# Kernel tuning notes

Hardware: AMD Instinct MI355X
Metric: run time of the kernel (lower is better)

The kernel has to match this reference:

```python
import jax, jax.numpy as jnp
import numpy as np
from math import factorial, sqrt, pi

MUL = 8
LS = [0, 1, 2]                       # l values for both Rs_in and Rs_out
RS = [(MUL, l) for l in LS]
N_NODES = 20000
N_EDGES = 100000
FEAT = sum(m * (2 * l + 1) for m, l in RS)       # 72
R_TOT = sum(mo * mi * (2 * min(lo, li) + 1) for mo, lo in RS for mi, li in RS)  # 1216
L_MAX = max(LS) + max(LS)            # 4
RSH_DIM = (L_MAX + 1) ** 2           # 25
NB, H = 10, 100                      # radial basis size / hidden width
MIN_R, MAX_R = 0.7, 3.2
SWISH_SCALE = 1.679177               # e3nn rescaled swish factor


def _w3j_entry(j1, j2, j3, m1, m2, m3):
    # complex-basis Wigner 3j (Racah formula)
    if m1 + m2 + m3 != 0 or not (abs(j1 - j2) <= j3 <= j1 + j2):
        return 0.0
    t1, t2 = j2 - m1 - j3, j1 + m2 - j3
    kmin, kmax = max(0, t1, t2), min(j1 + j2 - j3, j1 - m1, j2 + m2)
    s = sum((-1) ** k / (factorial(k) * factorial(k - t1) * factorial(k - t2)
                         * factorial(j1 + j2 - j3 - k) * factorial(j1 - m1 - k) * factorial(j2 + m2 - k))
            for k in range(kmin, kmax + 1))
    pref = (-1) ** (j1 - j2 - m3) * sqrt(
        factorial(j1 + j2 - j3) * factorial(j1 - j2 + j3) * factorial(-j1 + j2 + j3) / factorial(j1 + j2 + j3 + 1)
        * factorial(j1 + m1) * factorial(j1 - m1) * factorial(j2 + m2) * factorial(j2 - m2)
        * factorial(j3 + m3) * factorial(j3 - m3))
    return pref * s


def _real_cob(l):
    # complex->real spherical-harmonic change of basis
    U = np.zeros((2 * l + 1, 2 * l + 1), dtype=complex)
    U[l, l] = 1.0
    s = 1.0 / np.sqrt(2.0)
    for m in range(1, l + 1):
        U[l + m, l + m] = (-1) ** m * s
        U[l + m, l - m] = s
        U[l - m, l - m] = 1j * s
        U[l - m, l + m] = -1j * ((-1) ** m) * s
    return U


def _wigner3j_real(l1, l2, l3):
    w = np.zeros((2 * l1 + 1, 2 * l2 + 1, 2 * l3 + 1))
    for m1 in range(-l1, l1 + 1):
        for m2 in range(-l2, l2 + 1):
            m3 = -m1 - m2
            if abs(m3) <= l3:
                w[m1 + l1, m2 + l2, m3 + l3] = _w3j_entry(l1, l2, l3, m1, m2, m3)
    T = np.einsum('am,bn,cp,mnp->abc', _real_cob(l1), _real_cob(l2), _real_cob(l3), w.astype(complex))
    C = T.real if np.linalg.norm(T.real) >= np.linalg.norm(T.imag) else T.imag
    n = np.linalg.norm(C)
    return (C / n if n > 0 else C).astype(np.float32)


# precomputed constants (coupling coefficients + normalization), as in MinimalNetwork.__init__
C3 = {(lo, li, lf): jnp.asarray(_wigner3j_real(lo, li, lf))
      for _, lo in RS for _, li in RS for lf in range(abs(lo - li), lo + li + 1)}


def _norm_coef():
    nc = np.zeros((len(RS), len(RS)), dtype=np.float32)
    for i, (_, lo) in enumerate(RS):
        num = sum(mi * (2 * min(lo, li) + 1) for mi, li in RS)
        nc[i, :] = sqrt(4 * pi) * sqrt(2 * lo + 1) / sqrt(num)
    return jnp.asarray(nc)

NORM = _norm_coef()


def _swish(x):
    return SWISH_SCALE * x * jax.nn.sigmoid(x)


def _radial(r, Ws):
    # GaussianRadialModel: gaussian basis -> 3 hidden swish layers -> linear out
    centers = jnp.linspace(MIN_R, MAX_R, NB)
    sigma = (MAX_R - MIN_R) / (NB - 1)
    x = jnp.exp(-(((r[:, None] - centers) / sigma) ** 2))
    for W in Ws[:-1]:
        x = _swish(x @ (W / jnp.sqrt(jnp.asarray(W.shape[0], x.dtype))))
    W = Ws[-1]
    return x @ (W / jnp.sqrt(jnp.asarray(W.shape[0], x.dtype)))


def _tensor_message(F_src, rsh, R):
    # F_src: [E, FEAT] gathered source features; rsh: [E, 25]; R: [E, R_TOT]
    E = F_src.shape[0]
    f_offs = np.cumsum([0] + [m * (2 * l + 1) for m, l in RS])
    msgs, r_off = [], 0
    for i, (U, lo) in enumerate(RS):
        acc = jnp.zeros((E, U, 2 * lo + 1), F_src.dtype)
        for j, (V, li) in enumerate(RS):
            nlf = 2 * min(lo, li) + 1
            Rb = R[:, r_off:r_off + U * V * nlf].reshape(E, U, V, nlf)
            r_off += U * V * nlf
            Fb = F_src[:, f_offs[j]:f_offs[j + 1]].reshape(E, V, 2 * li + 1)
            for fi, lf in enumerate(range(abs(lo - li), lo + li + 1)):
                # K[e,mo,mi] = sum_mf C3[mo,mi,mf] * Y_lf[e,mf]
                K = jnp.einsum('oif,ef->eoi', C3[(lo, li, lf)], rsh[:, lf * lf:(lf + 1) * (lf + 1)])
                acc = acc + NORM[i, j] * jnp.einsum('eoi,evi,euv->euo', K, Fb, Rb[..., fi])
        msgs.append(acc.reshape(E, -1))
    return jnp.concatenate(msgs, axis=-1)


def _forward(features, edge_index, radii, rsh, Ws):
    R = _radial(radii, Ws)                                     # [E, R_TOT]
    msg = _tensor_message(features[edge_index[0]], rsh, R)     # [E, FEAT]
    # scatter-add aggregation at target nodes (MessagePassing aggr='add')
    return jnp.zeros((features.shape[0], msg.shape[1]), msg.dtype).at[edge_index[1]].add(msg)


def setup_inputs() -> dict:
    key = jax.random.key(0)
    ks = jax.random.split(key, 8)
    features = jax.random.normal(ks[0], (N_NODES, FEAT), jnp.float32)
    edge_index = jax.random.randint(ks[1], (2, N_EDGES), 0, N_NODES)
    radii = MIN_R + (MAX_R - MIN_R) * jax.random.uniform(ks[2], (N_EDGES,), jnp.float32)
    rsh = jax.random.normal(ks[3], (N_EDGES, RSH_DIM), jnp.float32)
    W0 = jax.random.normal(ks[4], (NB, H), jnp.float32)
    W1 = jax.random.normal(ks[5], (H, H), jnp.float32)
    W2 = jax.random.normal(ks[6], (H, H), jnp.float32)
    W3 = jax.random.normal(ks[7], (H, R_TOT), jnp.float32)
    return {"features": features, "edge_index": edge_index, "radii": radii, "rsh": rsh,
            "W0": W0, "W1": W1, "W2": W2, "W3": W3}


def reference(features, edge_index, radii, rsh, W0, W1, W2, W3):
    return _forward(features, edge_index, radii, rsh, (W0, W1, W2, W3))
```

## Files before the change

kernel.cpp:

```cpp
#include <hip/hip_runtime.h>
#include <hip/hip_bf16.h>
#include <math.h>


#define FEATD 72
#define NCOL 1216
#define SWISH_SCALE 1.679177f

typedef __attribute__((ext_vector_type(8))) short bf16x8;
typedef __attribute__((ext_vector_type(4))) float f32x4;

constexpr int NCOMBO = 19;
constexpr int CB_LO[NCOMBO] = {0,0,0,1,1,1,1,1,1,1,2,2,2,2,2,2,2,2,2};
constexpr int CB_LI[NCOMBO] = {0,1,2,0,1,1,1,2,2,2,0,1,1,1,2,2,2,2,2};
constexpr int CB_LF[NCOMBO] = {0,1,2,1,0,1,2,1,2,3,2,1,2,3,0,1,2,3,4};
constexpr int CB_OFF[NCOMBO] = {0,1,10,35,44,53,80,125,170,245,350,375,420,495,600,625,700,825,1000};
constexpr int CB_SZ[NCOMBO]  = {1,9,25,9,9,27,45,45,75,105,25,45,75,105,25,75,125,175,225};
constexpr int C3TOT = 1225;

constexpr int C3OFFT[3][3][5] = {
  { {0,-1,-1,-1,-1}, {-1,1,-1,-1,-1}, {-1,-1,10,-1,-1} },
  { {-1,35,-1,-1,-1}, {44,53,80,-1,-1}, {-1,125,170,245,-1} },
  { {-1,-1,350,-1,-1}, {-1,375,420,495,-1}, {600,625,700,825,1000} }
};
constexpr int ROFFT[3][3] = {{0,64,128},{192,256,448},{640,704,896}};
constexpr int FOFFT[3]   = {0,8,32};

__device__ const double d_fact[11] = {1.,1.,2.,6.,24.,120.,720.,5040.,40320.,362880.,3628800.};

__device__ double w3j_entry(int j1,int j2,int j3,int m1,int m2,int m3){
  if (m1+m2+m3 != 0) return 0.0;
  int dj = j1-j2; if (dj<0) dj=-dj;
  if (j3 < dj || j3 > j1+j2) return 0.0;
  int t1 = j2 - m1 - j3, t2 = j1 + m2 - j3;
  int kmin = 0; if (t1>kmin) kmin=t1; if (t2>kmin) kmin=t2;
  int kmax = j1+j2-j3; if (j1-m1<kmax) kmax=j1-m1; if (j2+m2<kmax) kmax=j2+m2;
  double s = 0.0;
  for (int k=kmin;k<=kmax;++k){
    double den = d_fact[k]*d_fact[k-t1]*d_fact[k-t2]*d_fact[j1+j2-j3-k]
               * d_fact[j1-m1-k]*d_fact[j2+m2-k];
    s += ((k&1)? -1.0:1.0)/den;
  }
  double pref = sqrt(d_fact[j1+j2-j3]*d_fact[j1-j2+j3]*d_fact[-j1+j2+j3]/d_fact[j1+j2+j3+1]
               * d_fact[j1+m1]*d_fact[j1-m1]*d_fact[j2+m2]*d_fact[j2-m2]
               * d_fact[j3+m3]*d_fact[j3-m3]);
  int ex = j1-j2-m3;
  if (ex & 1) pref = -pref;
  return pref*s;
}

__device__ void cob(int l, int r, int c, double& re, double& im){
  re = 0.0; im = 0.0;
  int mr = r - l, mc = c - l;
  const double s = 0.70710678118654752440;
  if (mr == 0) { if (mc == 0) re = 1.0; return; }
  if (mr > 0) {
    if (mc == mr)       re = (mr & 1) ? -s : s;
    else if (mc == -mr) re = s;
  } else {
    int m = -mr;
    if (mc == -m)      im = s;
    else if (mc == m)  im = (m & 1) ? s : -s;
  }
}

__global__ void c3_build_kernel(double* __restrict__ Tre, double* __restrict__ Tim){
  int idx = blockIdx.x*64 + threadIdx.x;
  if (idx >= C3TOT) return;
  int c = 0;
  while (c+1 < NCOMBO && idx >= CB_OFF[c+1]) ++c;
  int lo = CB_LO[c], li = CB_LI[c], lf = CB_LF[c];
  int n2 = 2*li+1, n3 = 2*lf+1;
  int loc = idx - CB_OFF[c];
  int a = loc/(n2*n3), b = (loc/n3)%n2, g = loc%n3;
  double sre=0.0, sim=0.0;
  for (int m1=-lo; m1<=lo; ++m1){
    for (int m2=-li; m2<=li; ++m2){
      int m3 = -m1-m2;
      if (m3 < -lf || m3 > lf) continue;
      double w = w3j_entry(lo,li,lf,m1,m2,m3);
      if (w == 0.0) continue;
      double r1,i1,r2,i2,r3,i3;
      cob(lo, a, m1+lo, r1,i1);
      cob(li, b, m2+li, r2,i2);
      cob(lf, g, m3+lf, r3,i3);
      double rr = r1*r2 - i1*i2, ri = r1*i2 + i1*r2;
      double fr = rr*r3 - ri*i3, fi = rr*i3 + ri*r3;
      sre += fr*w; sim += fi*w;
    }
  }
  Tre[idx] = sre; Tim[idx] = sim;
}

__global__ void c3_norm_kernel(const double* __restrict__ Tre, const double* __restrict__ Tim,
                               float* __restrict__ C3f){
  int c = blockIdx.x;
  int off = CB_OFF[c], sz = CB_SZ[c];
  int t = threadIdx.x;
  double sre=0.0, sim=0.0;
  for (int p=t; p<sz; p+=64){ double x=Tre[off+p], y=Tim[off+p]; sre+=x*x; sim+=y*y; }
  for (int m=1; m<64; m<<=1){ sre += __shfl_xor(sre, m, 64); sim += __shfl_xor(sim, m, 64); }
  bool useRe = (sre >= sim);
  double n = sqrt(useRe ? sre : sim);
  double inv = (n > 0.0) ? 1.0/n : 1.0;
  for (int p=t; p<sz; p+=64){
    double v = useRe ? Tre[off+p] : Tim[off+p];
    C3f[off+p] = (float)(v*inv);
  }
}

__global__ __launch_bounds__(256) void prep_w3t_kernel(const float* __restrict__ W3,
                                                       __hip_bfloat16* __restrict__ W3t){
  int idx = blockIdx.x*256 + threadIdx.x;
  if (idx >= 1216*136) return;
  int cp = idx/136, k = idx%136;
  int chunk = cp>>6, uv = cp&63;
  int lo = CB_LO[chunk], li = CB_LI[chunk], lf = CB_LF[chunk];
  int lmin = lo<li ? lo : li;
  int nlf = 2*lmin+1;
  int fi = lf - (lo>li ? lo-li : li-lo);
  int c = ROFFT[lo][li] + uv*nlf + fi;
  float v = (k < 100) ? 0.1f*W3[(size_t)k*NCOL + c] : 0.f;
  W3t[idx] = __float2bfloat16(v);
}

__global__ __launch_bounds__(256) void prep_wt_kernel(const float* __restrict__ W1,
                                                      const float* __restrict__ W2,
                                                      __hip_bfloat16* __restrict__ W1t,
                                                      __hip_bfloat16* __restrict__ W2t){
  int idx = blockIdx.x*256 + threadIdx.x;
  constexpr int HALF = 112*136;
  if (idx >= 2*HALF) return;
  const float* W = (idx < HALF) ? W1 : W2;
  __hip_bfloat16* Wt = (idx < HALF) ? W1t : W2t;
  int r = (idx < HALF) ? idx : idx - HALF;
  int o = r/136, k = r%136;
  float v = (o < 100 && k < 100) ? 0.1f*W[k*100+o] : 0.f;
  Wt[r] = __float2bfloat16(v);
}

__device__ __forceinline__ float swishf(float s){
  return SWISH_SCALE * s / (1.f + __expf(-s));
}

__device__ __forceinline__ void radial_layer_mfma(
    const __hip_bfloat16* __restrict__ sIn,
    const __hip_bfloat16* __restrict__ Wt,
    __hip_bfloat16* __restrict__ sOut,
    int wv, int lr, int lq)
{
  bf16x8 bf[4];
  #pragma unroll
  for (int ks=0; ks<4; ++ks)
    bf[ks] = *(const bf16x8*)&sIn[(wv*16+lr)*136 + ks*32 + lq*8];
  f32x4 acc[7] = {};
  #pragma unroll
  for (int ks=0; ks<4; ++ks)
    #pragma unroll
    for (int ot=0; ot<7; ++ot){
      bf16x8 a = *(const bf16x8*)&Wt[(ot*16+lr)*136 + ks*32 + lq*8];
      acc[ot] = __builtin_amdgcn_mfma_f32_16x16x32_bf16(a, bf[ks], acc[ot], 0, 0, 0);
    }
  #pragma unroll
  for (int ot=0; ot<7; ++ot){
    __hip_bfloat16 hv[4];
    #pragma unroll
    for (int r=0; r<4; ++r)
      hv[r] = __float2bfloat16(swishf(acc[ot][r]));
    *(short4*)&sOut[(wv*16+lr)*136 + ot*16 + lq*4] = *(short4*)hv;
  }
  {
    int lane = lq*16 + lr;
    int row = lane & 15, q = lane >> 4;
    short4 z = {0,0,0,0};
    *(short4*)&sOut[(wv*16+row)*136 + 112 + q*4] = z;
  }
}

__global__ __launch_bounds__(256,4) void radial_mfma_kernel(
    const float* __restrict__ radii, const float* __restrict__ W0,
    const __hip_bfloat16* __restrict__ W1t, const __hip_bfloat16* __restrict__ W2t,
    __hip_bfloat16* __restrict__ h_bf, int E)
{
  __shared__ float sbas[640];
  __shared__ __align__(16) __hip_bfloat16 sA[64*136];
  __shared__ __align__(16) __hip_bfloat16 sB[64*136];
  const int t = threadIdx.x;
  const int et0 = blockIdx.x*64;

  for (int p=t; p<640; p+=256){
    int er = p/10, k = p%10;
    int eg = et0 + er;
    float r = (eg < E) ? radii[eg] : 0.f;
    float c = 0.7f + (2.5f/9.0f)*(float)k;
    float d = (r - c) * (9.0f/2.5f);
    sbas[p] = __expf(-d*d);
  }
  __syncthreads();
  for (int p=t; p<6400; p+=256){
    int er = p/100, o = p%100;
    float s = 0.f;
    #pragma unroll
    for (int k=0;k<10;++k) s += sbas[er*10+k]*W0[k*100+o];
    sA[er*136+o] = __float2bfloat16(swishf(s*0.3162277660168379f));
  }
  for (int p=t; p<64*36; p+=256){
    int er = p/36, k = 100 + p%36;
    sA[er*136+k] = __float2bfloat16(0.f);
  }
  __syncthreads();

  const int lane = t & 63, wv = t >> 6;
  const int lr = lane & 15, lq = lane >> 4;

  radial_layer_mfma(sA, W1t, sB, wv, lr, lq);
  __builtin_amdgcn_wave_barrier();
  radial_layer_mfma(sB, W2t, sA, wv, lr, lq);
  __builtin_amdgcn_wave_barrier();
  {
    const float4* sm = (const float4*)(sA + (size_t)(wv*16)*136);
    float4* gm = (float4*)(h_bf + (size_t)(et0 + wv*16)*136);
    for (int p=lane; p<272; p+=64) gm[p] = sm[p];
  }
}

__global__ __launch_bounds__(256) void hist_kernel(const int* __restrict__ ei,
                                                   int* __restrict__ deg, int E){
  int e = blockIdx.x*256 + threadIdx.x;
  if (e < E) atomicAdd(&deg[ei[E+e]], 1);
}

__global__ __launch_bounds__(256) void scan_kernel(const int* __restrict__ deg,
                                                   int* __restrict__ off,
                                                   int* __restrict__ cursor, int N, int E){
  __shared__ int part[256], spref[256];
  const int t = threadIdx.x;
  const int CH = (N + 255)/256;
  int lo = t*CH, hi = lo+CH < N ? lo+CH : N;
  int s = 0;
  for (int n=lo; n<hi; ++n) s += deg[n];
  part[t] = s;
  __syncthreads();
  if (t == 0){
    int run = 0;
    for (int i=0;i<256;++i){ spref[i] = run; run += part[i]; }
  }
  __syncthreads();
  int run = spref[t];
  for (int n=lo; n<hi; ++n){ off[n] = run; cursor[n] = run; run += deg[n]; }
  if (t == 255) off[N] = E;
}

__global__ __launch_bounds__(256) void fill_kernel(const int* __restrict__ ei,
                                                   int* __restrict__ cursor,
                                                   int* __restrict__ eid, int E){
  int e = blockIdx.x*256 + threadIdx.x;
  if (e < E){
    int idx = atomicAdd(&cursor[ei[E+e]], 1);
    eid[idx] = e;
  }
}

__global__ __launch_bounds__(64) void gather_kernel(const float* __restrict__ msg,
                                                    const int* __restrict__ off,
                                                    const int* __restrict__ eid,
                                                    float* __restrict__ out, int N){
  const int n = blockIdx.x;
  const int t = threadIdx.x;
  const int s = off[n], e1 = off[n+1];
  float a0 = 0.f, a1 = 0.f;
  for (int i=s; i<e1; ++i){
    const float* m = msg + (size_t)eid[i]*FEATD;
    a0 += m[t];
    if (t < 8) a1 += m[64+t];
  }
  out[(size_t)n*FEATD + t] = a0;
  if (t < 8) out[(size_t)n*FEATD + 64 + t] = a1;
}

constexpr int OF_RT  = 0;
constexpr int OF_ACC = 17408;
constexpr int OF_F   = 27648;
constexpr int OF_KV  = 46080;
constexpr int OF_SRC = 52480;
constexpr int SMEM_SZ = 52736;

template<int LO,int LI,int LF>
__device__ __forceinline__ void phase(
    int chunk, const __hip_bfloat16* __restrict__ W3t, const bf16x8 (&hf)[4],
    float* sRt, float* sFf, float* sKV,
    const float* __restrict__ C3g, const float* __restrict__ rshrow,
    float* sAcc, int t)
{
  constexpr int NO = 2*LO+1, NI = 2*LI+1, NF = 2*LF+1;
  constexpr int C3B = C3OFFT[LO][LI][LF];
  constexpr int FO  = FOFFT[LI];

  const int e = t >> 2, role = t & 3;
  const int lane = t & 63, wv = t >> 6;
  const int lr = lane & 15, lq = lane >> 4;

  {
    float y[NF];
    #pragma unroll
    for (int mf=0; mf<NF; ++mf) y[mf] = rshrow[LF*LF + mf];
    for (int it = role; it < NO*NI; it += 4){
      float s = 0.f;
      #pragma unroll
      for (int mf=0; mf<NF; ++mf) s += C3g[C3B + it*NF + mf] * y[mf];
      sKV[e*25 + it] = s;
    }
  }
  {
    const __hip_bfloat16* wb = W3t + (size_t)chunk*64*136;
    f32x4 a4[4] = {};
    #pragma unroll
    for (int ks=0; ks<4; ++ks){
      #pragma unroll
      for (int ct=0; ct<4; ++ct){
        bf16x8 a = *(const bf16x8*)&wb[(ct*16+lr)*136 + ks*32 + lq*8];
        a4[ct] = __builtin_amdgcn_mfma_f32_16x16x32_bf16(a, hf[ks], a4[ct], 0, 0, 0);
      }
    }
    #pragma unroll
    for (int ct=0; ct<4; ++ct)
      *(f32x4*)&sRt[(wv*16 + lr)*68 + ct*16 + lq*4] = a4[ct];
  }
  __builtin_amdgcn_wave_barrier();

  {
    float H[2][NI];
    #pragma unroll
    for (int du=0; du<2; ++du)
      #pragma unroll
      for (int mi=0; mi<NI; ++mi) H[du][mi] = 0.f;

    #pragma unroll
    for (int vg=0; vg<2; ++vg){
      float fb[4*NI];
      #pragma unroll
      for (int p=0; p<NI; ++p)
        *(f32x4*)&fb[p*4] = *(const f32x4*)&sFf[e*72 + FO + vg*4*NI + p*4];
      #pragma unroll
      for (int du=0; du<2; ++du){
        const int u = role*2 + du;
        f32x4 rv = *(const f32x4*)&sRt[e*68 + u*8 + vg*4];
        #pragma unroll
        for (int v=0; v<4; ++v)
          #pragma unroll
          for (int mi=0; mi<NI; ++mi)
            H[du][mi] += rv[v] * fb[v*NI + mi];
      }
    }
    const int u0 = role*2, u1 = role*2 + 1;
    const int b0 = e*40 + ((LO==0) ? u0 : (LO==1) ? u0*3 : u0*5);
    const int b1 = e*40 + ((LO==0) ? u1 : (LO==1) ? u1*3 : u1*5);
    #pragma unroll
    for (int o=0; o<NO; ++o){
      float s0 = 0.f, s1 = 0.f;
      #pragma unroll
      for (int mi=0; mi<NI; ++mi){
        float kvv = sKV[e*25 + o*NI + mi];
        s0 += kvv * H[0][mi];
        s1 += kvv * H[1][mi];
      }
      sAcc[b0 + o] += s0;
      sAcc[b1 + o] += s1;
    }
  }
  __builtin_amdgcn_wave_barrier();
}

template<int J0,int W>
__device__ __forceinline__ void flush_group(float* sAcc, float* __restrict__ msg,
                                            int eb, int t, float nrm)
{
  const int lane = t & 63, wv = t >> 6;
  __builtin_amdgcn_wave_barrier();
  for (int p = lane; p < 16*W; p += 64){
    int el = wv*16 + p/W, j = p%W;
    msg[(size_t)(eb + el)*FEATD + J0 + j] = nrm * sAcc[el*40 + j];
    sAcc[el*40 + j] = 0.f;
  }
  __builtin_amdgcn_wave_barrier();
}

__global__ __launch_bounds__(256,3) void fused_kernel(
    const float* __restrict__ feats, const int* __restrict__ ei,
    const float* __restrict__ rsh, const __hip_bfloat16* __restrict__ h_bf,
    const __hip_bfloat16* __restrict__ W3t, const float* __restrict__ C3g,
    float* __restrict__ msg, int E)
{
  __shared__ __align__(16) char smem[SMEM_SZ];
  float* sRt  = (float*)(smem + OF_RT);
  float* sAcc = (float*)(smem + OF_ACC);
  float* sFf  = (float*)(smem + OF_F);
  float* sKV  = (float*)(smem + OF_KV);
  int*   sSrc = (int*)(smem + OF_SRC);

  const int t = threadIdx.x;
  const int eb = blockIdx.x*64;

  bf16x8 hf[4];
  {
    const int lane = t & 63, wv = t >> 6;
    const int lr = lane & 15, lq = lane >> 4;
    const __hip_bfloat16* hrow = h_bf + (size_t)(eb + wv*16 + lr)*136;
    #pragma unroll
    for (int ks=0; ks<4; ++ks)
      hf[ks] = *(const bf16x8*)&hrow[ks*32 + lq*8];
  }
  for (int p=t; p<2560; p+=256) sAcc[p] = 0.f;
  for (int p=t; p<64; p+=256){
    int e = eb + p;
    sSrc[p] = (e < E) ? ei[e] : 0;
  }
  __syncthreads();
  for (int p=t; p<64*72; p+=256){
    int el = p/72, j = p%72;
    sFf[el*72 + j] = feats[(size_t)sSrc[el]*72 + j];
  }
  __syncthreads();

  int eg = eb + (t >> 2); if (eg > E-1) eg = E-1;
  const float* rshrow = rsh + (size_t)eg*25;

  phase<0,0,0>( 0, W3t, hf, sRt, sFf, sKV, C3g, rshrow, sAcc, t);
  phase<0,1,1>( 1, W3t, hf, sRt, sFf, sKV, C3g, rshrow, sAcc, t);
  phase<0,2,2>( 2, W3t, hf, sRt, sFf, sKV, C3g, rshrow, sAcc, t);
  flush_group<0,8>(sAcc, msg, eb, t, 0.72360125f);

  phase<1,0,1>( 3, W3t, hf, sRt, sFf, sKV, C3g, rshrow, sAcc, t);
  phase<1,1,0>( 4, W3t, hf, sRt, sFf, sKV, C3g, rshrow, sAcc, t);
  phase<1,1,1>( 5, W3t, hf, sRt, sFf, sKV, C3g, rshrow, sAcc, t);
  phase<1,1,2>( 6, W3t, hf, sRt, sFf, sKV, C3g, rshrow, sAcc, t);
  phase<1,2,1>( 7, W3t, hf, sRt, sFf, sKV, C3g, rshrow, sAcc, t);
  phase<1,2,2>( 8, W3t, hf, sRt, sFf, sKV, C3g, rshrow, sAcc, t);
  phase<1,2,3>( 9, W3t, hf, sRt, sFf, sKV, C3g, rshrow, sAcc, t);
  flush_group<8,24>(sAcc, msg, eb, t, 0.8204867f);

  phase<2,0,2>(10, W3t, hf, sRt, sFf, sKV, C3g, rshrow, sAcc, t);
  phase<2,1,1>(11, W3t, hf, sRt, sFf, sKV, C3g, rshrow, sAcc, t);
  phase<2,1,2>(12, W3t, hf, sRt, sFf, sKV, C3g, rshrow, sAcc, t);
  phase<2,1,3>(13, W3t, hf, sRt, sFf, sKV, C3g, rshrow, sAcc, t);
  phase<2,2,0>(14, W3t, hf, sRt, sFf, sKV, C3g, rshrow, sAcc, t);
  phase<2,2,1>(15, W3t, hf, sRt, sFf, sKV, C3g, rshrow, sAcc, t);
  phase<2,2,2>(16, W3t, hf, sRt, sFf, sKV, C3g, rshrow, sAcc, t);
  phase<2,2,3>(17, W3t, hf, sRt, sFf, sKV, C3g, rshrow, sAcc, t);
  phase<2,2,4>(18, W3t, hf, sRt, sFf, sKV, C3g, rshrow, sAcc, t);
  flush_group<32,40>(sAcc, msg, eb, t, 0.9341652f);
}

extern "C" void kernel_launch(void* const* d_in, const int* in_sizes, int n_in,
                              void* d_out, int out_size, void* d_ws, size_t ws_size,
                              hipStream_t stream)
{
  const float* feats = (const float*)d_in[0];
  const int*   ei    = (const int*)d_in[1];
  const float* radii = (const float*)d_in[2];
  const float* rsh   = (const float*)d_in[3];
  const float* W0    = (const float*)d_in[4];
  const float* W1    = (const float*)d_in[5];
  const float* W2    = (const float*)d_in[6];
  const float* W3    = (const float*)d_in[7];
  float* out = (float*)d_out;
  const int E = in_sizes[2];
  const int N = in_sizes[0]/FEATD;

  const int EPAD = ((E + 63)/64)*64;
  const int NBLK = EPAD/64;

  char* ws = (char*)d_ws;
  size_t off_b = 0;
  float*  C3f = (float*)(ws + off_b);  off_b += 8192;
  double* Tre = (double*)(ws + off_b); off_b += 12288;
  double* Tim = (double*)(ws + off_b); off_b += 12288;
  __hip_bfloat16* W3t = (__hip_bfloat16*)(ws + off_b); off_b += 335872;
  __hip_bfloat16* W1t = (__hip_bfloat16*)(ws + off_b); off_b += 30720;
  __hip_bfloat16* W2t = (__hip_bfloat16*)(ws + off_b); off_b += 30720;
  __hip_bfloat16* h_bf = (__hip_bfloat16*)(ws + off_b); off_b += (size_t)EPAD*272;
  float* msg = (float*)(ws + off_b);   off_b += (size_t)EPAD*FEATD*4;
  int* deg    = (int*)(ws + off_b);    off_b += (size_t)N*4;
  int* offv   = (int*)(ws + off_b);    off_b += (size_t)(N+1)*4;
  int* cursor = (int*)(ws + off_b);    off_b += (size_t)N*4;
  int* eid    = (int*)(ws + off_b);    off_b += (size_t)E*4;

  c3_build_kernel<<<dim3((C3TOT+63)/64), dim3(64), 0, stream>>>(Tre, Tim);
  c3_norm_kernel<<<dim3(NCOMBO), dim3(64), 0, stream>>>(Tre, Tim, C3f);
  prep_w3t_kernel<<<dim3((1216*136+255)/256), dim3(256), 0, stream>>>(W3, W3t);
  prep_wt_kernel<<<dim3((2*112*136+255)/256), dim3(256), 0, stream>>>(W1, W2, W1t, W2t);

  hipMemsetAsync(deg, 0, (size_t)N*4, stream);
  hist_kernel<<<dim3((E+255)/256), dim3(256), 0, stream>>>(ei, deg, E);
  scan_kernel<<<dim3(1), dim3(256), 0, stream>>>(deg, offv, cursor, N, E);
  fill_kernel<<<dim3((E+255)/256), dim3(256), 0, stream>>>(ei, cursor, eid, E);

  radial_mfma_kernel<<<dim3(NBLK), dim3(256), 0, stream>>>(radii, W0, W1t, W2t, h_bf, E);
  fused_kernel<<<dim3(NBLK), dim3(256), 0, stream>>>(feats, ei, rsh, h_bf, W3t, C3f, msg, E);
  gather_kernel<<<dim3(N), dim3(64), 0, stream>>>(msg, offv, eid, out, N);
}
```

Measured before the change: 409.7 us.

## Stage W3 chunks into swizzled LDS via async global-to-LDS loads

Each phase now copies its 64x128 bf16 W3 chunk into shared memory with global_load_lds using an XOR-swizzled layout, and the MFMA A-fragments are read from LDS instead of global memory. The rsh rows and the C3 coefficients are also cached in shared memory once per block. The aim is to cut repeated global/L2 traffic and uncoalesced fragment loads, and to overlap the chunk copy with the KV computation. In exchange, two block-wide barriers are added per phase, LDS use grows to about 80 KB, and occupancy drops from 3 to 2 blocks per CU.

```diff
diff --git a/kernel.cpp b/kernel.cpp
--- a/kernel.cpp
+++ b/kernel.cpp
@@ -112,16 +112,17 @@
 __global__ __launch_bounds__(256) void prep_w3t_kernel(const float* __restrict__ W3,
                                                        __hip_bfloat16* __restrict__ W3t){
   int idx = blockIdx.x*256 + threadIdx.x;
-  if (idx >= 1216*136) return;
-  int cp = idx/136, k = idx%136;
-  int chunk = cp>>6, uv = cp&63;
+  if (idx >= 1216*128) return;
+  int cp = idx >> 7, k = idx & 127;
+  int chunk = cp >> 6, r = cp & 63;
   int lo = CB_LO[chunk], li = CB_LI[chunk], lf = CB_LF[chunk];
   int lmin = lo<li ? lo : li;
   int nlf = 2*lmin+1;
   int fi = lf - (lo>li ? lo-li : li-lo);
-  int c = ROFFT[lo][li] + uv*nlf + fi;
+  int c = ROFFT[lo][li] + r*nlf + fi;
   float v = (k < 100) ? 0.1f*W3[(size_t)k*NCOL + c] : 0.f;
-  W3t[idx] = __float2bfloat16(v);
+  int swz = (r*16 + (k>>3)) ^ (r&7);
+  W3t[(size_t)chunk*8192 + swz*8 + (k&7)] = __float2bfloat16(v);
 }
 
 __global__ __launch_bounds__(256) void prep_wt_kernel(const float* __restrict__ W1,
@@ -278,18 +279,35 @@
   if (t < 8) out[(size_t)n*FEATD + 64 + t] = a1;
 }
 
-constexpr int OF_RT  = 0;
-constexpr int OF_ACC = 17408;
-constexpr int OF_F   = 27648;
-constexpr int OF_KV  = 46080;
-constexpr int OF_SRC = 52480;
-constexpr int SMEM_SZ = 52736;
+constexpr int OF_W   = 0;
+constexpr int OF_RT  = 16384;
+constexpr int OF_ACC = 33792;
+constexpr int OF_F   = 44032;
+constexpr int OF_KV  = 62464;
+constexpr int OF_RSH = 68864;
+constexpr int OF_C3  = 75264;
+constexpr int OF_SRC = 80176;
+constexpr int SMEM_SZ = 80432;
+
+__device__ __forceinline__ void stage_chunk(const __hip_bfloat16* __restrict__ W3t,
+                                            int chunk, char* sW, int t)
+{
+  const int lane = t & 63, wv = t >> 6;
+  const char* g = (const char*)W3t + (size_t)chunk*16384;
+  #pragma unroll
+  for (int r=0; r<4; ++r){
+    const char* gsrc = g + (wv*256 + r*64 + lane)*16;
+    __builtin_amdgcn_global_load_lds(
+        (const __attribute__((address_space(1))) unsigned int*)gsrc,
+        (__attribute__((address_space(3))) unsigned int*)(sW + wv*4096 + r*1024),
+        16, 0, 0);
+  }
+}
 
 template<int LO,int LI,int LF>
 __device__ __forceinline__ void phase(
     int chunk, const __hip_bfloat16* __restrict__ W3t, const bf16x8 (&hf)[4],
-    float* sRt, float* sFf, float* sKV,
-    const float* __restrict__ C3g, const float* __restrict__ rshrow,
+    char* sW, float* sRt, float* sFf, float* sRsh, float* sKV, const float* sC3,
     float* sAcc, int t)
 {
   constexpr int NO = 2*LO+1, NI = 2*LI+1, NF = 2*LF+1;
@@ -300,25 +318,31 @@
   const int lane = t & 63, wv = t >> 6;
   const int lr = lane & 15, lq = lane >> 4;
 
+  __syncthreads();
+  stage_chunk(W3t, chunk, sW, t);
+
   {
     float y[NF];
     #pragma unroll
-    for (int mf=0; mf<NF; ++mf) y[mf] = rshrow[LF*LF + mf];
+    for (int mf=0; mf<NF; ++mf) y[mf] = sRsh[e*25 + LF*LF + mf];
     for (int it = role; it < NO*NI; it += 4){
       float s = 0.f;
       #pragma unroll
-      for (int mf=0; mf<NF; ++mf) s += C3g[C3B + it*NF + mf] * y[mf];
+      for (int mf=0; mf<NF; ++mf) s += sC3[C3B + it*NF + mf] * y[mf];
       sKV[e*25 + it] = s;
     }
   }
+  __syncthreads();
+
   {
-    const __hip_bfloat16* wb = W3t + (size_t)chunk*64*136;
     f32x4 a4[4] = {};
     #pragma unroll
     for (int ks=0; ks<4; ++ks){
       #pragma unroll
       for (int ct=0; ct<4; ++ct){
-        bf16x8 a = *(const bf16x8*)&wb[(ct*16+lr)*136 + ks*32 + lq*8];
+        const int row = ct*16 + lr;
+        const int u   = (row*16 + (ks*4 + lq)) ^ (row & 7);
+        bf16x8 a = *(const bf16x8*)(sW + u*16);
         a4[ct] = __builtin_amdgcn_mfma_f32_16x16x32_bf16(a, hf[ks], a4[ct], 0, 0, 0);
       }
     }
@@ -385,17 +409,20 @@
   __builtin_amdgcn_wave_barrier();
 }
 
-__global__ __launch_bounds__(256,3) void fused_kernel(
+__global__ __launch_bounds__(256,2) void fused_kernel(
     const float* __restrict__ feats, const int* __restrict__ ei,
     const float* __restrict__ rsh, const __hip_bfloat16* __restrict__ h_bf,
     const __hip_bfloat16* __restrict__ W3t, const float* __restrict__ C3g,
     float* __restrict__ msg, int E)
 {
   __shared__ __align__(16) char smem[SMEM_SZ];
+  char*  sW   = smem + OF_W;
   float* sRt  = (float*)(smem + OF_RT);
   float* sAcc = (float*)(smem + OF_ACC);
   float* sFf  = (float*)(smem + OF_F);
   float* sKV  = (float*)(smem + OF_KV);
+  float* sRsh = (float*)(smem + OF_RSH);
+  float* sC3  = (float*)(smem + OF_C3);
   int*   sSrc = (int*)(smem + OF_SRC);
 
   const int t = threadIdx.x;
@@ -415,6 +442,12 @@
     int e = eb + p;
     sSrc[p] = (e < E) ? ei[e] : 0;
   }
+  for (int p=t; p<1600; p+=256){
+    int el = p/25, j = p%25;
+    int e = eb + el;
+    sRsh[el*25 + j] = (e < E) ? rsh[(size_t)e*25 + j] : 0.f;
+  }
+  for (int p=t; p<C3TOT; p+=256) sC3[p] = C3g[p];
   __syncthreads();
   for (int p=t; p<64*72; p+=256){
     int el = p/72, j = p%72;
@@ -422,32 +455,29 @@
   }
   __syncthreads();
 
-  int eg = eb + (t >> 2); if (eg > E-1) eg = E-1;
-  const float* rshrow = rsh + (size_t)eg*25;
-
-  phase<0,0,0>( 0, W3t, hf, sRt, sFf, sKV, C3g, rshrow, sAcc, t);
-  phase<0,1,1>( 1, W3t, hf, sRt, sFf, sKV, C3g, rshrow, sAcc, t);
-  phase<0,2,2>( 2, W3t, hf, sRt, sFf, sKV, C3g, rshrow, sAcc, t);
+  phase<0,0,0>( 0, W3t, hf, sW, sRt, sFf, sRsh, sKV, sC3, sAcc, t);
+  phase<0,1,1>( 1, W3t, hf, sW, sRt, sFf, sRsh, sKV, sC3, sAcc, t);
+  phase<0,2,2>( 2, W3t, hf, sW, sRt, sFf, sRsh, sKV, sC3, sAcc, t);
   flush_group<0,8>(sAcc, msg, eb, t, 0.72360125f);
 
-  phase<1,0,1>( 3, W3t, hf, sRt, sFf, sKV, C3g, rshrow, sAcc, t);
-  phase<1,1,0>( 4, W3t, hf, sRt, sFf, sKV, C3g, rshrow, sAcc, t);
-  phase<1,1,1>( 5, W3t, hf, sRt, sFf, sKV, C3g, rshrow, sAcc, t);
-  phase<1,1,2>( 6, W3t, hf, sRt, sFf, sKV, C3g, rshrow, sAcc, t);
-  phase<1,2,1>( 7, W3t, hf, sRt, sFf, sKV, C3g, rshrow, sAcc, t);
-  phase<1,2,2>( 8, W3t, hf, sRt, sFf, sKV, C3g, rshrow, sAcc, t);
-  phase<1,2,3>( 9, W3t, hf, sRt, sFf, sKV, C3g, rshrow, sAcc, t);
+  phase<1,0,1>( 3, W3t, hf, sW, sRt, sFf, sRsh, sKV, sC3, sAcc, t);
+  phase<1,1,0>( 4, W3t, hf, sW, sRt, sFf, sRsh, sKV, sC3, sAcc, t);
+  phase<1,1,1>( 5, W3t, hf, sW, sRt, sFf, sRsh, sKV, sC3, sAcc, t);
+  phase<1,1,2>( 6, W3t, hf, sW, sRt, sFf, sRsh, sKV, sC3, sAcc, t);
+  phase<1,2,1>( 7, W3t, hf, sW, sRt, sFf, sRsh, sKV, sC3, sAcc, t);
+  phase<1,2,2>( 8, W3t, hf, sW, sRt, sFf, sRsh, sKV, sC3, sAcc, t);
+  phase<1,2,3>( 9, W3t, hf, sW, sRt, sFf, sRsh, sKV, sC3, sAcc, t);
   flush_group<8,24>(sAcc, msg, eb, t, 0.8204867f);
 
-  phase<2,0,2>(10, W3t, hf, sRt, sFf, sKV, C3g, rshrow, sAcc, t);
-  phase<2,1,1>(11, W3t, hf, sRt, sFf, sKV, C3g, rshrow, sAcc, t);
-  phase<2,1,2>(12, W3t, hf, sRt, sFf, sKV, C3g, rshrow, sAcc, t);
-  phase<2,1,3>(13, W3t, hf, sRt, sFf, sKV, C3g, rshrow, sAcc, t);
-  phase<2,2,0>(14, W3t, hf, sRt, sFf, sKV, C3g, rshrow, sAcc, t);
-  phase<2,2,1>(15, W3t, hf, sRt, sFf, sKV, C3g, rshrow, sAcc, t);
-  phase<2,2,2>(16, W3t, hf, sRt, sFf, sKV, C3g, rshrow, sAcc, t);
-  phase<2,2,3>(17, W3t, hf, sRt, sFf, sKV, C3g, rshrow, sAcc, t);
-  phase<2,2,4>(18, W3t, hf, sRt, sFf, sKV, C3g, rshrow, sAcc, t);
+  phase<2,0,2>(10, W3t, hf, sW, sRt, sFf, sRsh, sKV, sC3, sAcc, t);
+  phase<2,1,1>(11, W3t, hf, sW, sRt, sFf, sRsh, sKV, sC3, sAcc, t);
+  phase<2,1,2>(12, W3t, hf, sW, sRt, sFf, sRsh, sKV, sC3, sAcc, t);
+  phase<2,1,3>(13, W3t, hf, sW, sRt, sFf, sRsh, sKV, sC3, sAcc, t);
+  phase<2,2,0>(14, W3t, hf, sW, sRt, sFf, sRsh, sKV, sC3, sAcc, t);
+  phase<2,2,1>(15, W3t, hf, sW, sRt, sFf, sRsh, sKV, sC3, sAcc, t);
+  phase<2,2,2>(16, W3t, hf, sW, sRt, sFf, sRsh, sKV, sC3, sAcc, t);
+  phase<2,2,3>(17, W3t, hf, sW, sRt, sFf, sRsh, sKV, sC3, sAcc, t);
+  phase<2,2,4>(18, W3t, hf, sW, sRt, sFf, sRsh, sKV, sC3, sAcc, t);
   flush_group<32,40>(sAcc, msg, eb, t, 0.9341652f);
 }
 
@@ -487,7 +517,7 @@
 
   c3_build_kernel<<<dim3((C3TOT+63)/64), dim3(64), 0, stream>>>(Tre, Tim);
   c3_norm_kernel<<<dim3(NCOMBO), dim3(64), 0, stream>>>(Tre, Tim, C3f);
-  prep_w3t_kernel<<<dim3((1216*136+255)/256), dim3(256), 0, stream>>>(W3, W3t);
+  prep_w3t_kernel<<<dim3((1216*128+255)/256), dim3(256), 0, stream>>>(W3, W3t);
   prep_wt_kernel<<<dim3((2*112*136+255)/256), dim3(256), 0, stream>>>(W1, W2, W1t, W2t);
 
   hipMemsetAsync(deg, 0, (size_t)N*4, stream);
```

After: 373.2 us. -8.9%, faster.
